# Performance work log

Measured on AMD Instinct MI355X. Metric: run time of the kernel, lower is better.

Reference implementation:

```python
import jax, jax.numpy as jnp
import numpy as np

B, S, T = 32, 512, 64
DENC = 1024   # encoder dim == dhid
DHID = 1024
DEMB = 512
V = 32000
NEG = 1e20


def setup_inputs() -> dict:
    key = jax.random.key(0)
    ks = jax.random.split(key, 13)
    u = lambda k, shape, a: jax.random.uniform(k, shape, jnp.float32, -a, a)
    klstm = 1.0 / np.sqrt(DHID)
    kproj = 1.0 / np.sqrt(DENC + DHID)
    return {
        "enc": jax.random.normal(ks[0], (B, S, DENC), jnp.float32),
        "inp_mask": jnp.ones((B, S), jnp.float32),
        "label": jax.random.randint(ks[1], (B, T), 0, V),
        "emb_w": jax.random.normal(ks[2], (V, DEMB), jnp.float32) * 0.02,
        "W_ih": u(ks[3], (4 * DHID, DENC + DEMB), klstm),
        "b_ih": u(ks[4], (4 * DHID,), klstm),
        "W_hh": u(ks[5], (4 * DHID, DHID), klstm),
        "b_hh": u(ks[6], (4 * DHID,), klstm),
        "proj_W": u(ks[7], (DEMB, DENC + DHID), kproj),
        "proj_b": u(ks[8], (DEMB,), kproj),
        "emb0": u(ks[9], (DEMB,), 0.1),
        "h0": u(ks[10], (DHID,), 0.1),
        "c0": u(ks[11], (DHID,), 0.1),
    }


def reference(enc, inp_mask, label, emb_w, W_ih, b_ih, W_hh, b_hh,
              proj_W, proj_b, emb0, h0, c0):
    batch = enc.shape[0]
    vocab = emb_w.shape[0]
    h = jnp.broadcast_to(h0, (batch, h0.shape[0]))
    c = jnp.broadcast_to(c0, (batch, c0.shape[0]))
    e = jnp.broadcast_to(emb0, (batch, emb0.shape[0]))
    neg_mask = (1.0 - inp_mask) * NEG  # [B, S]
    emb_T = jax.lax.stop_gradient(emb_w).T  # detached vocab projection

    def step(carry, label_t):
        h, c, e = carry
        # attention over encoder states keyed by h
        score = jnp.einsum('bsd,bd->bs', enc, h) - neg_mask
        attn = jax.nn.softmax(score, axis=1)
        ctx = jnp.einsum('bs,bsd->bd', attn, enc)  # [B, DENC]
        # LSTMCell (torch gate order: i, f, g, o)
        x = jnp.concatenate([ctx, e], axis=1)
        gates = x @ W_ih.T + b_ih + h @ W_hh.T + b_hh
        i, f, g, o = jnp.split(gates, 4, axis=1)
        c = jax.nn.sigmoid(f) * c + jax.nn.sigmoid(i) * jnp.tanh(g)
        h = jax.nn.sigmoid(o) * jnp.tanh(c)
        # project to embedding space, score against vocab
        p = jnp.concatenate([ctx, h], axis=1) @ proj_W.T + proj_b
        out = p @ emb_T  # [B, V]
        # teacher forcing: next input embedding from label
        word = jnp.clip(label_t, 0, vocab - 1)
        e = emb_w[word]
        return (h, c, e), out

    _, outs = jax.lax.scan(step, (h, c, e), label.T)  # outs: [T, B, V]
    return jnp.transpose(outs, (1, 0, 2))  # [B, T, V]
```

## Files before the change

kernel.cpp:

```cpp
#include <hip/hip_runtime.h>
#include <hip/hip_bf16.h>


#define B_   32
#define S_   512
#define T_   64
#define DENC 1024
#define DHID 1024
#define DEMB 512
#define V_   32000
#define KX   2560
#define KP   2048
#define NCH  32

using short8 = __attribute__((ext_vector_type(8))) short;
using f32x4  = __attribute__((ext_vector_type(4))) float;
typedef __hip_bfloat16 bf16;

__device__ __forceinline__ float sigmoidf_(float x) { return 1.0f / (1.0f + expf(-x)); }
__device__ __forceinline__ bf16 bhi(float x) { return __float2bfloat16(x); }
__device__ __forceinline__ bf16 blo(float x) {
    return __float2bfloat16(x - __bfloat162float(__float2bfloat16(x)));
}

#define MFMA(a, b, c) __builtin_amdgcn_mfma_f32_16x16x32_bf16((a), (b), (c), 0, 0, 0)
#define DOT4(a, b) fmaf((a).x, (b).x, fmaf((a).y, (b).y, fmaf((a).z, (b).z, (a).w * (b).w)))


__global__ void k_build_wg(const float* __restrict__ W_ih, const float* __restrict__ W_hh,
                           const float* __restrict__ b_ih, const float* __restrict__ b_hh,
                           bf16* __restrict__ Wh, bf16* __restrict__ Wl, float* __restrict__ bias) {
    int jp = blockIdx.x;
    int g = jp & 3, d = jp >> 2;
    int j = g * 1024 + d;
    const float* wi = W_ih + (size_t)j * 1536;
    const float* wh = W_hh + (size_t)j * 1024;
    bf16* dh = Wh + (size_t)jp * KX;
    bf16* dl = Wl + (size_t)jp * KX;
    for (int i = threadIdx.x; i < 1024; i += 256) { float v = wi[i];      dh[i] = bhi(v);        dl[i] = blo(v); }
    for (int i = threadIdx.x; i < 1024; i += 256) { float v = wh[i];      dh[1024+i] = bhi(v);   dl[1024+i] = blo(v); }
    for (int i = threadIdx.x; i < 512;  i += 256) { float v = wi[1024+i]; dh[2048+i] = bhi(v);   dl[2048+i] = blo(v); }
    if (threadIdx.x == 0) bias[jp] = b_ih[j] + b_hh[j];
}

__global__ void k_cvt(const float* __restrict__ src, bf16* __restrict__ dst, long n) {
    long i = (long)blockIdx.x * blockDim.x + threadIdx.x;
    long stride = (long)gridDim.x * blockDim.x;
    for (; i < n; i += stride) dst[i] = __float2bfloat16(src[i]);
}

__global__ void k_cvt_split(const float* __restrict__ src, bf16* __restrict__ dh,
                            bf16* __restrict__ dl, long n) {
    long i = (long)blockIdx.x * blockDim.x + threadIdx.x;
    long stride = (long)gridDim.x * blockDim.x;
    for (; i < n; i += stride) { float v = src[i]; dh[i] = bhi(v); dl[i] = blo(v); }
}

__global__ void k_init(const float* __restrict__ h0, const float* __restrict__ c0,
                       const float* __restrict__ emb0,
                       float* __restrict__ h, float* __restrict__ c,
                       bf16* __restrict__ Hh, bf16* __restrict__ Hl,
                       bf16* __restrict__ Xh_, bf16* __restrict__ Xl_) {
    int b = blockIdx.x;
    for (int d = threadIdx.x; d < 1024; d += 256) {
        float v = h0[d];
        h[b * 1024 + d] = v;
        c[b * 1024 + d] = c0[d];
        Hh[b * 1024 + d] = bhi(v);
        Hl[b * 1024 + d] = blo(v);
    }
    for (int d = threadIdx.x; d < 512; d += 256) {
        float v = emb0[d];
        Xh_[(size_t)b * KX + 2048 + d] = bhi(v);
        Xl_[(size_t)b * KX + 2048 + d] = blo(v);
    }
}


__global__ __launch_bounds__(256) void k_att(
    const float* __restrict__ enc, const float* __restrict__ mask,
    const float* __restrict__ h,
    bf16* __restrict__ Xh_, bf16* __restrict__ Xl_,
    const bf16* __restrict__ Hh, const bf16* __restrict__ Hl,
    const bf16* __restrict__ PWh, const bf16* __restrict__ PWl,
    const float* __restrict__ pb, const float* __restrict__ emb_w,
    const int* __restrict__ label,
    bf16* __restrict__ Ph, bf16* __restrict__ Pl,
    float* __restrict__ pml, float* __restrict__ pctx, int t)
{
    __shared__ float pr[4][32][17];
    __shared__ float lctx[4][1024];
    __shared__ float lm[4], ll[4];

    int bid = blockIdx.x;
    int tid = threadIdx.x, wave = tid >> 6, lane = tid & 63;

    if (bid < 32) {
        if (t == 0) return;
        int tp = t - 1;
        int nb = bid * 16;
        int ncol = nb + (lane & 15);
        int kc = wave * 512;
        const short* ah;
        const short* al;
        size_t astr, aoff;
        if (wave < 2) { ah = (const short*)Xh_; al = (const short*)Xl_; astr = KX;   aoff = kc; }
        else          { ah = (const short*)Hh;  al = (const short*)Hl;  astr = 1024; aoff = kc - 1024; }
        const short* wrh = (const short*)PWh + (size_t)ncol * KP + kc + (lane >> 4) * 8;
        const short* wrl = (const short*)PWl + (size_t)ncol * KP + kc + (lane >> 4) * 8;
        size_t arow0 = (size_t)(lane & 15) * astr + aoff + (lane >> 4) * 8;
        size_t arow1 = (size_t)((lane & 15) + 16) * astr + aoff + (lane >> 4) * 8;
        f32x4 acc0 = {0, 0, 0, 0}, acc1 = {0, 0, 0, 0};
#pragma unroll 4
        for (int kk = 0; kk < 16; ++kk) {
            int ko = kk * 32;
            short8 a0h = *(const short8*)(ah + arow0 + ko);
            short8 a1h = *(const short8*)(ah + arow1 + ko);
            short8 a0l = *(const short8*)(al + arow0 + ko);
            short8 a1l = *(const short8*)(al + arow1 + ko);
            short8 bh = *(const short8*)(wrh + ko);
            short8 bl = *(const short8*)(wrl + ko);
            acc0 = MFMA(a0h, bh, acc0); acc1 = MFMA(a1h, bh, acc1);
            acc0 = MFMA(a0h, bl, acc0); acc1 = MFMA(a1h, bl, acc1);
            acc0 = MFMA(a0l, bh, acc0); acc1 = MFMA(a1l, bh, acc1);
        }
#pragma unroll
        for (int r = 0; r < 4; ++r) {
            pr[wave][(lane >> 4) * 4 + r][lane & 15]      = acc0[r];
            pr[wave][16 + (lane >> 4) * 4 + r][lane & 15] = acc1[r];
        }
        __syncthreads();
        for (int p = tid; p < 512; p += 256) {
            int bb = p >> 4, col = p & 15;
            float v = pr[0][bb][col] + pr[1][bb][col] + pr[2][bb][col] + pr[3][bb][col]
                      + pb[nb + col];
            size_t mi = (size_t)(bb * 64 + tp) * 512 + nb + col;
            Ph[mi] = bhi(v);
            Pl[mi] = blo(v);
        }
        int b = bid;
        int wd = label[b * 64 + tp];
        wd = wd < 0 ? 0 : (wd > V_ - 1 ? V_ - 1 : wd);
        const float* ew = emb_w + (size_t)wd * 512;
        for (int d = tid; d < 512; d += 256) {
            float v = ew[d];
            Xh_[(size_t)b * KX + 2048 + d] = bhi(v);
            Xl_[(size_t)b * KX + 2048 + d] = blo(v);
        }
        return;
    }

    if (t >= T_) return;
    int ab = bid - 32;
    int b = ab >> 5, ch = ab & (NCH - 1);

    float4 hreg[4];
    const float4* h4p = (const float4*)(h + b * 1024);
#pragma unroll
    for (int j = 0; j < 4; ++j) hreg[j] = h4p[j * 64 + lane];

    const float* encb = enc + (size_t)b * S_ * DENC;
    int srow0 = ch * 16 + wave * 4;
    const float4* r0 = (const float4*)(encb + (size_t)(srow0 + 0) * DENC);
    const float4* r1 = (const float4*)(encb + (size_t)(srow0 + 1) * DENC);
    const float4* r2 = (const float4*)(encb + (size_t)(srow0 + 2) * DENC);
    const float4* r3 = (const float4*)(encb + (size_t)(srow0 + 3) * DENC);
    float4 e00 = r0[lane], e01 = r0[64+lane], e02 = r0[128+lane], e03 = r0[192+lane];
    float4 e10 = r1[lane], e11 = r1[64+lane], e12 = r1[128+lane], e13 = r1[192+lane];
    float4 e20 = r2[lane], e21 = r2[64+lane], e22 = r2[128+lane], e23 = r2[192+lane];
    float4 e30 = r3[lane], e31 = r3[64+lane], e32 = r3[128+lane], e33 = r3[192+lane];

    float d0 = DOT4(e00,hreg[0]) + DOT4(e01,hreg[1]) + DOT4(e02,hreg[2]) + DOT4(e03,hreg[3]);
    float d1 = DOT4(e10,hreg[0]) + DOT4(e11,hreg[1]) + DOT4(e12,hreg[2]) + DOT4(e13,hreg[3]);
    float d2 = DOT4(e20,hreg[0]) + DOT4(e21,hreg[1]) + DOT4(e22,hreg[2]) + DOT4(e23,hreg[3]);
    float d3 = DOT4(e30,hreg[0]) + DOT4(e31,hreg[1]) + DOT4(e32,hreg[2]) + DOT4(e33,hreg[3]);
#pragma unroll
    for (int off = 32; off; off >>= 1) {
        d0 += __shfl_xor(d0, off, 64);
        d1 += __shfl_xor(d1, off, 64);
        d2 += __shfl_xor(d2, off, 64);
        d3 += __shfl_xor(d3, off, 64);
    }
    float sc0 = d0 - (1.0f - mask[b * S_ + srow0 + 0]) * 1e20f;
    float sc1 = d1 - (1.0f - mask[b * S_ + srow0 + 1]) * 1e20f;
    float sc2 = d2 - (1.0f - mask[b * S_ + srow0 + 2]) * 1e20f;
    float sc3 = d3 - (1.0f - mask[b * S_ + srow0 + 3]) * 1e20f;
    float mw = fmaxf(fmaxf(sc0, sc1), fmaxf(sc2, sc3));
    float w0 = expf(sc0 - mw), w1 = expf(sc1 - mw);
    float w2 = expf(sc2 - mw), w3 = expf(sc3 - mw);
    float lw = w0 + w1 + w2 + w3;
    float4 c0, c1, c2, c3;
    c0.x = w0*e00.x + w1*e10.x + w2*e20.x + w3*e30.x;
    c0.y = w0*e00.y + w1*e10.y + w2*e20.y + w3*e30.y;
    c0.z = w0*e00.z + w1*e10.z + w2*e20.z + w3*e30.z;
    c0.w = w0*e00.w + w1*e10.w + w2*e20.w + w3*e30.w;
    c1.x = w0*e01.x + w1*e11.x + w2*e21.x + w3*e31.x;
    c1.y = w0*e01.y + w1*e11.y + w2*e21.y + w3*e31.y;
    c1.z = w0*e01.z + w1*e11.z + w2*e21.z + w3*e31.z;
    c1.w = w0*e01.w + w1*e11.w + w2*e21.w + w3*e31.w;
    c2.x = w0*e02.x + w1*e12.x + w2*e22.x + w3*e32.x;
    c2.y = w0*e02.y + w1*e12.y + w2*e22.y + w3*e32.y;
    c2.z = w0*e02.z + w1*e12.z + w2*e22.z + w3*e32.z;
    c2.w = w0*e02.w + w1*e12.w + w2*e22.w + w3*e32.w;
    c3.x = w0*e03.x + w1*e13.x + w2*e23.x + w3*e33.x;
    c3.y = w0*e03.y + w1*e13.y + w2*e23.y + w3*e33.y;
    c3.z = w0*e03.z + w1*e13.z + w2*e23.z + w3*e33.z;
    c3.w = w0*e03.w + w1*e13.w + w2*e23.w + w3*e33.w;

    ((float4*)lctx[wave])[0 * 64 + lane] = c0;
    ((float4*)lctx[wave])[1 * 64 + lane] = c1;
    ((float4*)lctx[wave])[2 * 64 + lane] = c2;
    ((float4*)lctx[wave])[3 * 64 + lane] = c3;
    if (lane == 0) { lm[wave] = mw; ll[wave] = lw; }
    __syncthreads();

    float mb_ = fmaxf(fmaxf(lm[0], lm[1]), fmaxf(lm[2], lm[3]));
    float q0 = expf(lm[0] - mb_), q1 = expf(lm[1] - mb_);
    float q2 = expf(lm[2] - mb_), q3 = expf(lm[3] - mb_);
    float lb = ll[0] * q0 + ll[1] * q1 + ll[2] * q2 + ll[3] * q3;
    float4 a0 = ((float4*)lctx[0])[tid], a1 = ((float4*)lctx[1])[tid];
    float4 a2 = ((float4*)lctx[2])[tid], a3 = ((float4*)lctx[3])[tid];
    float4 v;
    v.x = a0.x * q0 + a1.x * q1 + a2.x * q2 + a3.x * q3;
    v.y = a0.y * q0 + a1.y * q1 + a2.y * q2 + a3.y * q3;
    v.z = a0.z * q0 + a1.z * q1 + a2.z * q2 + a3.z * q3;
    v.w = a0.w * q0 + a1.w * q1 + a2.w * q2 + a3.w * q3;
    int pi = b * NCH + ch;
    ((float4*)(pctx + (size_t)pi * 1024))[tid] = v;
    if (tid == 0) { pml[pi * 2] = mb_; pml[pi * 2 + 1] = lb; }
}


__global__ __launch_bounds__(256) void k_comb(const float* __restrict__ pml,
                                              const float* __restrict__ pctx,
                                              const bf16* __restrict__ Hh,
                                              const bf16* __restrict__ Hl,
                                              bf16* __restrict__ Xh_, bf16* __restrict__ Xl_) {
    __shared__ float sml[NCH * 2];
    __shared__ float wch[NCH];
    int b = blockIdx.x, tid = threadIdx.x;
    if (tid < NCH * 2) sml[tid] = pml[b * NCH * 2 + tid];
    __syncthreads();
    float mf = -3.0e38f;
#pragma unroll
    for (int c = 0; c < NCH; ++c) mf = fmaxf(mf, sml[2 * c]);
    float lt = 0.f;
#pragma unroll
    for (int c = 0; c < NCH; ++c) lt += sml[2 * c + 1] * expf(sml[2 * c] - mf);
    if (tid < NCH) wch[tid] = expf(sml[2 * tid] - mf);
    __syncthreads();
    float inv = 1.0f / lt;
    const float4* base = (const float4*)(pctx + (size_t)b * NCH * 1024) + tid;
    float4 sacc = {0, 0, 0, 0};
#pragma unroll 8
    for (int c = 0; c < NCH; ++c) {
        float wc = wch[c];
        float4 p = base[c * 256];
        sacc.x = fmaf(wc, p.x, sacc.x); sacc.y = fmaf(wc, p.y, sacc.y);
        sacc.z = fmaf(wc, p.z, sacc.z); sacc.w = fmaf(wc, p.w, sacc.w);
    }
    sacc.x *= inv; sacc.y *= inv; sacc.z *= inv; sacc.w *= inv;
    size_t xi = (size_t)b * KX + tid * 4;
    Xh_[xi + 0] = bhi(sacc.x); Xl_[xi + 0] = blo(sacc.x);
    Xh_[xi + 1] = bhi(sacc.y); Xl_[xi + 1] = blo(sacc.y);
    Xh_[xi + 2] = bhi(sacc.z); Xl_[xi + 2] = blo(sacc.z);
    Xh_[xi + 3] = bhi(sacc.w); Xl_[xi + 3] = blo(sacc.w);
    ((unsigned long long*)(Xh_ + (size_t)b * KX + 1024))[tid] =
        ((const unsigned long long*)(Hh + (size_t)b * 1024))[tid];
    ((unsigned long long*)(Xl_ + (size_t)b * KX + 1024))[tid] =
        ((const unsigned long long*)(Hl + (size_t)b * 1024))[tid];
}


__global__ __launch_bounds__(256) void k_gates(
    const bf16* __restrict__ Xh_, const bf16* __restrict__ Xl_,
    const bf16* __restrict__ Wh_, const bf16* __restrict__ Wl_,
    const float* __restrict__ bias,
    float* __restrict__ c, float* __restrict__ h,
    bf16* __restrict__ Hh, bf16* __restrict__ Hl)
{
    __shared__ float pr[4][32][17];
    int jb = blockIdx.x * 16;
    int tid = threadIdx.x, wave = tid >> 6, lane = tid & 63;
    int jcol = jb + (lane & 15);
    int kc = wave * 640 + (lane >> 4) * 8;
    const short* xhp = (const short*)Xh_ + kc;
    const short* xlp = (const short*)Xl_ + kc;
    const short* wrh = (const short*)Wh_ + (size_t)jcol * KX + kc;
    const short* wrl = (const short*)Wl_ + (size_t)jcol * KX + kc;
    size_t arow0 = (size_t)(lane & 15) * KX;
    size_t arow1 = (size_t)((lane & 15) + 16) * KX;
    f32x4 acc0 = {0, 0, 0, 0}, acc1 = {0, 0, 0, 0};
#pragma unroll 4
    for (int kk = 0; kk < 20; ++kk) {
        int ko = kk * 32;
        short8 a0h = *(const short8*)(xhp + arow0 + ko);
        short8 a1h = *(const short8*)(xhp + arow1 + ko);
        short8 a0l = *(const short8*)(xlp + arow0 + ko);
        short8 a1l = *(const short8*)(xlp + arow1 + ko);
        short8 bh = *(const short8*)(wrh + ko);
        short8 bl = *(const short8*)(wrl + ko);
        acc0 = MFMA(a0h, bh, acc0); acc1 = MFMA(a1h, bh, acc1);
        acc0 = MFMA(a0h, bl, acc0); acc1 = MFMA(a1h, bl, acc1);
        acc0 = MFMA(a0l, bh, acc0); acc1 = MFMA(a1l, bh, acc1);
    }
#pragma unroll
    for (int r = 0; r < 4; ++r) {
        pr[wave][(lane >> 4) * 4 + r][lane & 15]      = acc0[r];
        pr[wave][16 + (lane >> 4) * 4 + r][lane & 15] = acc1[r];
    }
    __syncthreads();
    if (tid < 128) {
        int bb = tid & 31, dd = tid >> 5;
        int cb = dd * 4;
        float gi = pr[0][bb][cb+0] + pr[1][bb][cb+0] + pr[2][bb][cb+0] + pr[3][bb][cb+0] + bias[jb+cb+0];
        float gf = pr[0][bb][cb+1] + pr[1][bb][cb+1] + pr[2][bb][cb+1] + pr[3][bb][cb+1] + bias[jb+cb+1];
        float gg = pr[0][bb][cb+2] + pr[1][bb][cb+2] + pr[2][bb][cb+2] + pr[3][bb][cb+2] + bias[jb+cb+2];
        float go = pr[0][bb][cb+3] + pr[1][bb][cb+3] + pr[2][bb][cb+3] + pr[3][bb][cb+3] + bias[jb+cb+3];
        int d = (jb >> 2) + dd;
        float cv = c[bb * 1024 + d];
        float cn = sigmoidf_(gf) * cv + sigmoidf_(gi) * tanhf(gg);
        float hn = sigmoidf_(go) * tanhf(cn);
        c[bb * 1024 + d] = cn;
        h[bb * 1024 + d] = hn;
        Hh[bb * 1024 + d] = bhi(hn);
        Hl[bb * 1024 + d] = blo(hn);
    }
}


__global__ __launch_bounds__(256) void k_out(const bf16* __restrict__ Ph,
                                             const bf16* __restrict__ Pl,
                                             const bf16* __restrict__ Eb,
                                             float* __restrict__ out) {
    int bid = blockIdx.x;
    int vb = (bid >> 4) * 128;
    int mb = (bid & 15) * 128;

    __shared__ __align__(16) short Ah[128][36];
    __shared__ __align__(16) short Al[128][36];
    __shared__ __align__(16) short Bs[128][36];

    int tid = threadIdx.x, wave = tid >> 6, lane = tid & 63;
    int wr = (wave >> 1) * 64, wc = (wave & 1) * 64;
    int fr = lane & 15, kg = lane >> 4;

    f32x4 acc[4][4];
#pragma unroll
    for (int m = 0; m < 4; ++m)
#pragma unroll
        for (int n = 0; n < 4; ++n) acc[m][n] = (f32x4){0, 0, 0, 0};

    const short* Pp = (const short*)Ph;
    const short* Plp = (const short*)Pl;
    const short* Ep = (const short*)Eb;

    for (int ks = 0; ks < 16; ++ks) {
        int k0 = ks * 32;
        __syncthreads();
#pragma unroll
        for (int j = 0; j < 2; ++j) {
            int cch = tid + j * 256;
            int r = cch >> 2, cg = (cch & 3) * 8;
            *(short8*)&Ah[r][cg] = *(const short8*)(Pp  + (size_t)(mb + r) * 512 + k0 + cg);
            *(short8*)&Al[r][cg] = *(const short8*)(Plp + (size_t)(mb + r) * 512 + k0 + cg);
            *(short8*)&Bs[r][cg] = *(const short8*)(Ep  + (size_t)(vb + r) * 512 + k0 + cg);
        }
        __syncthreads();
        short8 afh[4], afl[4], bf_[4];
#pragma unroll
        for (int m = 0; m < 4; ++m) {
            afh[m] = *(const short8*)&Ah[wr + m * 16 + fr][kg * 8];
            afl[m] = *(const short8*)&Al[wr + m * 16 + fr][kg * 8];
        }
#pragma unroll
        for (int n = 0; n < 4; ++n)
            bf_[n] = *(const short8*)&Bs[wc + n * 16 + fr][kg * 8];
#pragma unroll
        for (int m = 0; m < 4; ++m)
#pragma unroll
            for (int n = 0; n < 4; ++n) {
                acc[m][n] = MFMA(afh[m], bf_[n], acc[m][n]);
                acc[m][n] = MFMA(afl[m], bf_[n], acc[m][n]);
            }
    }
#pragma unroll
    for (int m = 0; m < 4; ++m)
#pragma unroll
        for (int n = 0; n < 4; ++n)
#pragma unroll
            for (int r = 0; r < 4; ++r) {
                int mm = mb + wr + m * 16 + kg * 4 + r;
                int vv = vb + wc + n * 16 + fr;
                __builtin_nontemporal_store(acc[m][n][r], &out[(size_t)mm * V_ + vv]);
            }
}


extern "C" void kernel_launch(void* const* d_in, const int* in_sizes, int n_in,
                              void* d_out, int out_size, void* d_ws, size_t ws_size,
                              hipStream_t stream) {
    (void)in_sizes; (void)n_in; (void)out_size; (void)ws_size;
    const float* enc    = (const float*)d_in[0];
    const float* mask   = (const float*)d_in[1];
    const int*   label  = (const int*)d_in[2];
    const float* emb_w  = (const float*)d_in[3];
    const float* W_ih   = (const float*)d_in[4];
    const float* b_ih   = (const float*)d_in[5];
    const float* W_hh   = (const float*)d_in[6];
    const float* b_hh   = (const float*)d_in[7];
    const float* proj_W = (const float*)d_in[8];
    const float* proj_b = (const float*)d_in[9];
    const float* emb0   = (const float*)d_in[10];
    const float* h0     = (const float*)d_in[11];
    const float* c0     = (const float*)d_in[12];
    float* out = (float*)d_out;

    char* w = (char*)d_ws;
    size_t o = 0;
    bf16* Wgh  = (bf16*)(w + o); o += (size_t)4096 * KX * 2;
    bf16* Wgl  = (bf16*)(w + o); o += (size_t)4096 * KX * 2;
    bf16* PWh  = (bf16*)(w + o); o += (size_t)512 * KP * 2;
    bf16* PWl  = (bf16*)(w + o); o += (size_t)512 * KP * 2;
    bf16* Eb   = (bf16*)(w + o); o += (size_t)V_ * 512 * 2;
    float* bias= (float*)(w + o); o += 4096 * 4;
    bf16* Xh   = (bf16*)(w + o); o += (size_t)32 * KX * 2;
    bf16* Xl   = (bf16*)(w + o); o += (size_t)32 * KX * 2;
    bf16* Hh   = (bf16*)(w + o); o += (size_t)32 * 1024 * 2;
    bf16* Hl   = (bf16*)(w + o); o += (size_t)32 * 1024 * 2;
    bf16* Ph   = (bf16*)(w + o); o += (size_t)2048 * 512 * 2;
    bf16* Pl   = (bf16*)(w + o); o += (size_t)2048 * 512 * 2;
    float* hb  = (float*)(w + o); o += (size_t)32 * 1024 * 4;
    float* cb  = (float*)(w + o); o += (size_t)32 * 1024 * 4;
    float* pml = (float*)(w + o); o += (size_t)32 * NCH * 2 * 4;
    float* pctx= (float*)(w + o); o += (size_t)32 * NCH * 1024 * 4;

    k_build_wg<<<4096, 256, 0, stream>>>(W_ih, W_hh, b_ih, b_hh, Wgh, Wgl, bias);
    k_cvt_split<<<1024, 256, 0, stream>>>(proj_W, PWh, PWl, (long)512 * KP);
    k_cvt<<<8192, 256, 0, stream>>>(emb_w, Eb, (long)V_ * 512);
    k_init<<<32, 256, 0, stream>>>(h0, c0, emb0, hb, cb, Hh, Hl, Xh, Xl);

    for (int t = 0; t <= T_; ++t) {
        k_att<<<32 + 32 * NCH, 256, 0, stream>>>(enc, mask, hb, Xh, Xl, Hh, Hl,
                                                 PWh, PWl, proj_b, emb_w, label,
                                                 Ph, Pl, pml, pctx, t);
        if (t < T_) {
            k_comb<<<32, 256, 0, stream>>>(pml, pctx, Hh, Hl, Xh, Xl);
            k_gates<<<256, 256, 0, stream>>>(Xh, Xl, Wgh, Wgl, bias, cb, hb, Hh, Hl);
        }
    }
    k_out<<<4000, 256, 0, stream>>>(Ph, Pl, Eb, out);
}
```

Measured before the change: 3.334 ms.

## Halve attention chunks with online softmax, widen gate split-K, pad LDS

The attention kernel now uses 16 chunks per batch row instead of 32, and each wave processes 8 encoder rows in two halves merged with an online-softmax rescale. This halves the partial contexts written and later combined, at the cost of fewer blocks and more work per wave. The gates kernel doubles to 512 threads with 8-way split-K, so each wave has a shorter K loop and the partial sums are reduced over 8 slices. The output GEMM's shared-memory row padding changes from 36 to 44 shorts, aimed at reducing bank conflicts.

New measurement: 2.822 ms. 1.18x faster.

```diff
diff --git a/kernel.cpp b/kernel.cpp
--- a/kernel.cpp
+++ b/kernel.cpp
@@ -11,7 +11,7 @@
 #define V_   32000
 #define KX   2560
 #define KP   2048
-#define NCH  32
+#define NCH  16
 
 using short8 = __attribute__((ext_vector_type(8))) short;
 using f32x4  = __attribute__((ext_vector_type(4))) float;
@@ -152,7 +152,7 @@
 
     if (t >= T_) return;
     int ab = bid - 32;
-    int b = ab >> 5, ch = ab & (NCH - 1);
+    int b = ab >> 4, ch = ab & (NCH - 1);
 
     float4 hreg[4];
     const float4* h4p = (const float4*)(h + b * 1024);
@@ -160,58 +160,68 @@
     for (int j = 0; j < 4; ++j) hreg[j] = h4p[j * 64 + lane];
 
     const float* encb = enc + (size_t)b * S_ * DENC;
-    int srow0 = ch * 16 + wave * 4;
-    const float4* r0 = (const float4*)(encb + (size_t)(srow0 + 0) * DENC);
-    const float4* r1 = (const float4*)(encb + (size_t)(srow0 + 1) * DENC);
-    const float4* r2 = (const float4*)(encb + (size_t)(srow0 + 2) * DENC);
-    const float4* r3 = (const float4*)(encb + (size_t)(srow0 + 3) * DENC);
-    float4 e00 = r0[lane], e01 = r0[64+lane], e02 = r0[128+lane], e03 = r0[192+lane];
-    float4 e10 = r1[lane], e11 = r1[64+lane], e12 = r1[128+lane], e13 = r1[192+lane];
-    float4 e20 = r2[lane], e21 = r2[64+lane], e22 = r2[128+lane], e23 = r2[192+lane];
-    float4 e30 = r3[lane], e31 = r3[64+lane], e32 = r3[128+lane], e33 = r3[192+lane];
-
-    float d0 = DOT4(e00,hreg[0]) + DOT4(e01,hreg[1]) + DOT4(e02,hreg[2]) + DOT4(e03,hreg[3]);
-    float d1 = DOT4(e10,hreg[0]) + DOT4(e11,hreg[1]) + DOT4(e12,hreg[2]) + DOT4(e13,hreg[3]);
-    float d2 = DOT4(e20,hreg[0]) + DOT4(e21,hreg[1]) + DOT4(e22,hreg[2]) + DOT4(e23,hreg[3]);
-    float d3 = DOT4(e30,hreg[0]) + DOT4(e31,hreg[1]) + DOT4(e32,hreg[2]) + DOT4(e33,hreg[3]);
-#pragma unroll
-    for (int off = 32; off; off >>= 1) {
-        d0 += __shfl_xor(d0, off, 64);
-        d1 += __shfl_xor(d1, off, 64);
-        d2 += __shfl_xor(d2, off, 64);
-        d3 += __shfl_xor(d3, off, 64);
-    }
-    float sc0 = d0 - (1.0f - mask[b * S_ + srow0 + 0]) * 1e20f;
-    float sc1 = d1 - (1.0f - mask[b * S_ + srow0 + 1]) * 1e20f;
-    float sc2 = d2 - (1.0f - mask[b * S_ + srow0 + 2]) * 1e20f;
-    float sc3 = d3 - (1.0f - mask[b * S_ + srow0 + 3]) * 1e20f;
-    float mw = fmaxf(fmaxf(sc0, sc1), fmaxf(sc2, sc3));
-    float w0 = expf(sc0 - mw), w1 = expf(sc1 - mw);
-    float w2 = expf(sc2 - mw), w3 = expf(sc3 - mw);
-    float lw = w0 + w1 + w2 + w3;
-    float4 c0, c1, c2, c3;
-    c0.x = w0*e00.x + w1*e10.x + w2*e20.x + w3*e30.x;
-    c0.y = w0*e00.y + w1*e10.y + w2*e20.y + w3*e30.y;
-    c0.z = w0*e00.z + w1*e10.z + w2*e20.z + w3*e30.z;
-    c0.w = w0*e00.w + w1*e10.w + w2*e20.w + w3*e30.w;
-    c1.x = w0*e01.x + w1*e11.x + w2*e21.x + w3*e31.x;
-    c1.y = w0*e01.y + w1*e11.y + w2*e21.y + w3*e31.y;
-    c1.z = w0*e01.z + w1*e11.z + w2*e21.z + w3*e31.z;
-    c1.w = w0*e01.w + w1*e11.w + w2*e21.w + w3*e31.w;
-    c2.x = w0*e02.x + w1*e12.x + w2*e22.x + w3*e32.x;
-    c2.y = w0*e02.y + w1*e12.y + w2*e22.y + w3*e32.y;
-    c2.z = w0*e02.z + w1*e12.z + w2*e22.z + w3*e32.z;
-    c2.w = w0*e02.w + w1*e12.w + w2*e22.w + w3*e32.w;
-    c3.x = w0*e03.x + w1*e13.x + w2*e23.x + w3*e33.x;
-    c3.y = w0*e03.y + w1*e13.y + w2*e23.y + w3*e33.y;
-    c3.z = w0*e03.z + w1*e13.z + w2*e23.z + w3*e33.z;
-    c3.w = w0*e03.w + w1*e13.w + w2*e23.w + w3*e33.w;
+    int srow0 = ch * 32 + wave * 8;
+
+    float m = -3.0e38f, l = 0.f;
+    float4 c0 = {0,0,0,0}, c1 = {0,0,0,0}, c2 = {0,0,0,0}, c3 = {0,0,0,0};
+#pragma unroll
+    for (int half = 0; half < 2; ++half) {
+        int sr = srow0 + half * 4;
+        const float4* r0 = (const float4*)(encb + (size_t)(sr + 0) * DENC);
+        const float4* r1 = (const float4*)(encb + (size_t)(sr + 1) * DENC);
+        const float4* r2 = (const float4*)(encb + (size_t)(sr + 2) * DENC);
+        const float4* r3 = (const float4*)(encb + (size_t)(sr + 3) * DENC);
+        float4 e00 = r0[lane], e01 = r0[64+lane], e02 = r0[128+lane], e03 = r0[192+lane];
+        float4 e10 = r1[lane], e11 = r1[64+lane], e12 = r1[128+lane], e13 = r1[192+lane];
+        float4 e20 = r2[lane], e21 = r2[64+lane], e22 = r2[128+lane], e23 = r2[192+lane];
+        float4 e30 = r3[lane], e31 = r3[64+lane], e32 = r3[128+lane], e33 = r3[192+lane];
+
+        float d0 = DOT4(e00,hreg[0]) + DOT4(e01,hreg[1]) + DOT4(e02,hreg[2]) + DOT4(e03,hreg[3]);
+        float d1 = DOT4(e10,hreg[0]) + DOT4(e11,hreg[1]) + DOT4(e12,hreg[2]) + DOT4(e13,hreg[3]);
+        float d2 = DOT4(e20,hreg[0]) + DOT4(e21,hreg[1]) + DOT4(e22,hreg[2]) + DOT4(e23,hreg[3]);
+        float d3 = DOT4(e30,hreg[0]) + DOT4(e31,hreg[1]) + DOT4(e32,hreg[2]) + DOT4(e33,hreg[3]);
+#pragma unroll
+        for (int off = 32; off; off >>= 1) {
+            d0 += __shfl_xor(d0, off, 64);
+            d1 += __shfl_xor(d1, off, 64);
+            d2 += __shfl_xor(d2, off, 64);
+            d3 += __shfl_xor(d3, off, 64);
+        }
+        float sc0 = d0 - (1.0f - mask[b * S_ + sr + 0]) * 1e20f;
+        float sc1 = d1 - (1.0f - mask[b * S_ + sr + 1]) * 1e20f;
+        float sc2 = d2 - (1.0f - mask[b * S_ + sr + 2]) * 1e20f;
+        float sc3 = d3 - (1.0f - mask[b * S_ + sr + 3]) * 1e20f;
+        float mw = fmaxf(fmaxf(sc0, sc1), fmaxf(sc2, sc3));
+        float mn = fmaxf(m, mw);
+        float f = expf(m - mn);
+        float g = expf(mw - mn);
+        float w0 = expf(sc0 - mw) * g, w1 = expf(sc1 - mw) * g;
+        float w2 = expf(sc2 - mw) * g, w3 = expf(sc3 - mw) * g;
+        l = l * f + (w0 + w1 + w2 + w3);
+        c0.x = c0.x * f + w0*e00.x + w1*e10.x + w2*e20.x + w3*e30.x;
+        c0.y = c0.y * f + w0*e00.y + w1*e10.y + w2*e20.y + w3*e30.y;
+        c0.z = c0.z * f + w0*e00.z + w1*e10.z + w2*e20.z + w3*e30.z;
+        c0.w = c0.w * f + w0*e00.w + w1*e10.w + w2*e20.w + w3*e30.w;
+        c1.x = c1.x * f + w0*e01.x + w1*e11.x + w2*e21.x + w3*e31.x;
+        c1.y = c1.y * f + w0*e01.y + w1*e11.y + w2*e21.y + w3*e31.y;
+        c1.z = c1.z * f + w0*e01.z + w1*e11.z + w2*e21.z + w3*e31.z;
+        c1.w = c1.w * f + w0*e01.w + w1*e11.w + w2*e21.w + w3*e31.w;
+        c2.x = c2.x * f + w0*e02.x + w1*e12.x + w2*e22.x + w3*e32.x;
+        c2.y = c2.y * f + w0*e02.y + w1*e12.y + w2*e22.y + w3*e32.y;
+        c2.z = c2.z * f + w0*e02.z + w1*e12.z + w2*e22.z + w3*e32.z;
+        c2.w = c2.w * f + w0*e02.w + w1*e12.w + w2*e22.w + w3*e32.w;
+        c3.x = c3.x * f + w0*e03.x + w1*e13.x + w2*e23.x + w3*e33.x;
+        c3.y = c3.y * f + w0*e03.y + w1*e13.y + w2*e23.y + w3*e33.y;
+        c3.z = c3.z * f + w0*e03.z + w1*e13.z + w2*e23.z + w3*e33.z;
+        c3.w = c3.w * f + w0*e03.w + w1*e13.w + w2*e23.w + w3*e33.w;
+        m = mn;
+    }
 
     ((float4*)lctx[wave])[0 * 64 + lane] = c0;
     ((float4*)lctx[wave])[1 * 64 + lane] = c1;
     ((float4*)lctx[wave])[2 * 64 + lane] = c2;
     ((float4*)lctx[wave])[3 * 64 + lane] = c3;
-    if (lane == 0) { lm[wave] = mw; ll[wave] = lw; }
+    if (lane == 0) { lm[wave] = m; ll[wave] = l; }
     __syncthreads();
 
     float mb_ = fmaxf(fmaxf(lm[0], lm[1]), fmaxf(lm[2], lm[3]));
@@ -272,18 +282,18 @@
 }
 
 
-__global__ __launch_bounds__(256) void k_gates(
+__global__ __launch_bounds__(512) void k_gates(
     const bf16* __restrict__ Xh_, const bf16* __restrict__ Xl_,
     const bf16* __restrict__ Wh_, const bf16* __restrict__ Wl_,
     const float* __restrict__ bias,
     float* __restrict__ c, float* __restrict__ h,
     bf16* __restrict__ Hh, bf16* __restrict__ Hl)
 {
-    __shared__ float pr[4][32][17];
+    __shared__ float pr[8][32][17];
     int jb = blockIdx.x * 16;
     int tid = threadIdx.x, wave = tid >> 6, lane = tid & 63;
     int jcol = jb + (lane & 15);
-    int kc = wave * 640 + (lane >> 4) * 8;
+    int kc = wave * 320 + (lane >> 4) * 8;
     const short* xhp = (const short*)Xh_ + kc;
     const short* xlp = (const short*)Xl_ + kc;
     const short* wrh = (const short*)Wh_ + (size_t)jcol * KX + kc;
@@ -291,8 +301,8 @@
     size_t arow0 = (size_t)(lane & 15) * KX;
     size_t arow1 = (size_t)((lane & 15) + 16) * KX;
     f32x4 acc0 = {0, 0, 0, 0}, acc1 = {0, 0, 0, 0};
-#pragma unroll 4
-    for (int kk = 0; kk < 20; ++kk) {
+#pragma unroll 5
+    for (int kk = 0; kk < 10; ++kk) {
         int ko = kk * 32;
         short8 a0h = *(const short8*)(xhp + arow0 + ko);
         short8 a1h = *(const short8*)(xhp + arow1 + ko);
@@ -313,10 +323,18 @@
     if (tid < 128) {
         int bb = tid & 31, dd = tid >> 5;
         int cb = dd * 4;
-        float gi = pr[0][bb][cb+0] + pr[1][bb][cb+0] + pr[2][bb][cb+0] + pr[3][bb][cb+0] + bias[jb+cb+0];
-        float gf = pr[0][bb][cb+1] + pr[1][bb][cb+1] + pr[2][bb][cb+1] + pr[3][bb][cb+1] + bias[jb+cb+1];
-        float gg = pr[0][bb][cb+2] + pr[1][bb][cb+2] + pr[2][bb][cb+2] + pr[3][bb][cb+2] + bias[jb+cb+2];
-        float go = pr[0][bb][cb+3] + pr[1][bb][cb+3] + pr[2][bb][cb+3] + pr[3][bb][cb+3] + bias[jb+cb+3];
+        float g0 = 0.f, g1 = 0.f, g2 = 0.f, g3 = 0.f;
+#pragma unroll
+        for (int q = 0; q < 8; ++q) {
+            g0 += pr[q][bb][cb + 0];
+            g1 += pr[q][bb][cb + 1];
+            g2 += pr[q][bb][cb + 2];
+            g3 += pr[q][bb][cb + 3];
+        }
+        float gi = g0 + bias[jb + cb + 0];
+        float gf = g1 + bias[jb + cb + 1];
+        float gg = g2 + bias[jb + cb + 2];
+        float go = g3 + bias[jb + cb + 3];
         int d = (jb >> 2) + dd;
         float cv = c[bb * 1024 + d];
         float cn = sigmoidf_(gf) * cv + sigmoidf_(gi) * tanhf(gg);
@@ -337,9 +355,9 @@
     int vb = (bid >> 4) * 128;
     int mb = (bid & 15) * 128;
 
-    __shared__ __align__(16) short Ah[128][36];
-    __shared__ __align__(16) short Al[128][36];
-    __shared__ __align__(16) short Bs[128][36];
+    __shared__ __align__(16) short Ah[128][44];
+    __shared__ __align__(16) short Al[128][44];
+    __shared__ __align__(16) short Bs[128][44];
 
     int tid = threadIdx.x, wave = tid >> 6, lane = tid & 63;
     int wr = (wave >> 1) * 64, wc = (wave & 1) * 64;
@@ -446,7 +464,7 @@
                                                  Ph, Pl, pml, pctx, t);
         if (t < T_) {
             k_comb<<<32, 256, 0, stream>>>(pml, pctx, Hh, Hl, Xh, Xl);
-            k_gates<<<256, 256, 0, stream>>>(Xh, Xl, Wgh, Wgl, bias, cb, hb, Hh, Hl);
+            k_gates<<<256, 512, 0, stream>>>(Xh, Xl, Wgh, Wgl, bias, cb, hb, Hh, Hl);
         }
     }
     k_out<<<4000, 256, 0, stream>>>(Ph, Pl, Eb, out);
```
